# Performance work log

Measured on AMD Instinct MI355X. Metric: run time of the kernel, lower is better.

The kernel has to match this reference:

```python
import jax, jax.numpy as jnp
import numpy as np

T, B = 128, 4096          # rollout length, num parallel envs
H = 128                   # lstm hidden
FEAT = 96                 # 32 (image) + 32 (loc) + 32 (energy)
NA = 6                    # num_actions
GRID, MAXE = 10.0, 200.0


def setup_inputs() -> dict:
    key = jax.random.key(0)
    ks = jax.random.split(key, 24)
    N = T * B
    w = lambda k, shp, s=0.05: (jax.random.normal(k, shp, jnp.float32) * s)
    return {
        "image": jax.random.uniform(ks[0], (N, 5, 5), jnp.float32),
        "location": jax.random.uniform(ks[1], (N, 2), jnp.float32),
        "energy": jax.random.uniform(ks[2], (N, 1), jnp.float32),
        "done": jax.random.randint(ks[3], (N,), 0, 2).astype(jnp.int32),
        "h0": jnp.zeros((B, H), jnp.float32),
        "c0": jnp.zeros((B, H), jnp.float32),
        # visual encoder MLP 25->256->256->128->32
        "W1": w(ks[4], (25, 256)),  "b1": jnp.zeros(256, jnp.float32),
        "W2": w(ks[5], (256, 256)), "b2": jnp.zeros(256, jnp.float32),
        "W3": w(ks[6], (256, 128)), "b3": jnp.zeros(128, jnp.float32),
        "W4": w(ks[7], (128, 32)),  "b4": jnp.zeros(32, jnp.float32),
        # location / energy encoders
        "Wl": w(ks[8], (2, 32)), "bl": jnp.zeros(32, jnp.float32),
        "We": w(ks[9], (1, 32)), "be": jnp.zeros(32, jnp.float32),
        # LSTM (PyTorch layout: gates [i,f,g,o], W_ih: [4H, in], W_hh: [4H, H])
        "Wih": w(ks[10], (4 * H, FEAT)), "Whh": w(ks[11], (4 * H, H)),
        "bih": jnp.zeros(4 * H, jnp.float32), "bhh": jnp.zeros(4 * H, jnp.float32),
        # actor / critic heads
        "Wa": w(ks[12], (H, NA)), "ba": jnp.zeros(NA, jnp.float32),
        "Wc": w(ks[13], (H, 1)),  "bc": jnp.zeros(1, jnp.float32),
    }


def _forward(image, location, energy, done, h0, c0,
             W1, b1, W2, b2, W3, b3, W4, b4, Wl, bl, We, be,
             Wih, Whh, bih, bhh, Wa, ba, Wc, bc):
    relu = jax.nn.relu
    x = image.reshape(-1, 25) / 255.0                      # [N,25]
    f = relu(x @ W1 + b1)
    f = relu(f @ W2 + b2)
    f = relu(f @ W3 + b3)
    img_feat = relu(f @ W4 + b4)                           # [N,32]
    loc_feat = (location / GRID) @ Wl + bl                 # [N,32]
    eng_feat = (energy / MAXE) @ We + be                   # [N,32]
    feats = jnp.concatenate([img_feat, loc_feat, eng_feat], axis=1)  # [N,96]
    xs = feats.reshape(T, B, FEAT)
    ds = done.astype(jnp.float32).reshape(T, B)
    bias = bih + bhh                                       # [4H]

    def step(carry, inp):
        h, c = carry                                       # [B,H]
        x_t, d_t = inp
        mask = (1.0 - d_t)[:, None]                        # reset on done
        h = h * mask
        c = c * mask
        gates = x_t @ Wih.T + h @ Whh.T + bias             # [B,4H]
        i, fg, g, o = jnp.split(gates, 4, axis=1)
        c = jax.nn.sigmoid(fg) * c + jax.nn.sigmoid(i) * jnp.tanh(g)
        h = jax.nn.sigmoid(o) * jnp.tanh(c)
        return (h, c), h

    (hT, cT), hs = jax.lax.scan(step, (h0, c0), (xs, ds))  # hs: [T,B,H]
    hidden = hs.reshape(-1, H)                             # [N,H]
    logits = hidden @ Wa + ba                              # [N,NA]
    value = hidden @ Wc + bc                               # [N,1]
    return jnp.concatenate([logits, value], axis=1)        # [N,NA+1]


def reference(image, location, energy, done, h0, c0,
              W1, b1, W2, b2, W3, b3, W4, b4, Wl, bl, We, be,
              Wih, Whh, bih, bhh, Wa, ba, Wc, bc):
    return _forward(image, location, energy, done, h0, c0,
                    W1, b1, W2, b2, W3, b3, W4, b4, Wl, bl, We, be,
                    Wih, Whh, bih, bhh, Wa, ba, Wc, bc)
```

## Files before the change

### kernel.cpp

```cpp
#include <hip/hip_runtime.h>

#define T_ 128
#define B_ 4096
#define N_ (T_*B_)
#define H_ 128
#define FEAT_ 96
#define K_ 224
#define G4H_ 512
#define L2E 1.4426950408889634f

typedef __attribute__((ext_vector_type(8))) short short8;
typedef __attribute__((ext_vector_type(4))) short short4v;
typedef __attribute__((ext_vector_type(4))) float f32x4;

__device__ __forceinline__ void bar_lgkm() {
    asm volatile("s_waitcnt lgkmcnt(0)\n\ts_barrier" ::: "memory");
}

__device__ __forceinline__ short f2bf(float f) {
    unsigned r;
    asm("v_cvt_pk_bf16_f32 %0, %1, %2" : "=v"(r) : "v"(f), "v"(f));
    return (short)(r & 0xffff);
}
__device__ __forceinline__ short4v pack4relu(const f32x4 a) {
    const float x0 = fmaxf(a[0], 0.f), x1 = fmaxf(a[1], 0.f);
    const float x2 = fmaxf(a[2], 0.f), x3 = fmaxf(a[3], 0.f);
    unsigned r01, r23;
    asm("v_cvt_pk_bf16_f32 %0, %1, %2" : "=v"(r01) : "v"(x0), "v"(x1));
    asm("v_cvt_pk_bf16_f32 %0, %1, %2" : "=v"(r23) : "v"(x2), "v"(x3));
    uint2 u; u.x = r01; u.y = r23;
    return __builtin_bit_cast(short4v, u);
}

#define FBASE(t, grp, kk) ((((size_t)(t) * 256 + (grp)) * 3 + (kk)) * 512)

__global__ __launch_bounds__(256) void prep_kernel(
    const float* __restrict__ Wih, const float* __restrict__ Whh,
    const float* __restrict__ bih, const float* __restrict__ bhh,
    const float* __restrict__ W1, const float* __restrict__ W2,
    const float* __restrict__ W3, const float* __restrict__ W4,
    short* __restrict__ Wtp, float* __restrict__ bias,
    short* __restrict__ W1p, short* __restrict__ W2p,
    short* __restrict__ W3p, short* __restrict__ W4p)
{
    int idx = blockIdx.x * 256 + threadIdx.x;
    if (idx < 114688) {
        int j = idx & 7, L = (idx >> 3) & 63, r = idx >> 9;
        int kk = r % 7, n = r / 7;
        int k = kk * 32 + ((L >> 4) << 3) + j;
        int g = (n << 4) + (L & 15);
        float v = (k < FEAT_) ? Wih[g * FEAT_ + k] : Whh[g * H_ + (k - FEAT_)];
        float s = (n >= 16 && n < 24) ? (2.0f * L2E) : L2E;
        Wtp[idx] = f2bf(v * s);
        return;
    }
    int e = idx - 114688;
    if (e < 8192) {
        int j = e & 7, L = (e >> 3) & 63, nt = e >> 9;
        int k = ((L >> 4) << 3) + j;
        int o = nt * 16 + (L & 15);
        W1p[e] = (k < 25) ? f2bf(W1[k * 256 + o] * (1.0f / 255.0f)) : (short)0;
        return;
    }
    e -= 8192;
    if (e < 65536) {
        int j = e & 7, L = (e >> 3) & 63, f = e >> 9;
        int kk = f & 7, nt = f >> 3;
        int k = kk * 32 + ((L >> 4) << 3) + j;
        W2p[e] = f2bf(W2[k * 256 + nt * 16 + (L & 15)]);
        return;
    }
    e -= 65536;
    if (e < 32768) {
        int j = e & 7, L = (e >> 3) & 63, f = e >> 9;
        int kk = f & 7, nt = f >> 3;
        int k = kk * 32 + ((L >> 4) << 3) + j;
        W3p[e] = f2bf(W3[k * 128 + nt * 16 + (L & 15)]);
        return;
    }
    e -= 32768;
    if (e < 4096) {
        int j = e & 7, L = (e >> 3) & 63, f = e >> 9;
        int kk = f & 3, nt = f >> 2;
        int k = kk * 32 + ((L >> 4) << 3) + j;
        W4p[e] = f2bf(W4[k * 32 + nt * 16 + (L & 15)]);
        return;
    }
    e -= 4096;
    if (e < 512) {
        float s = ((e >> 7) == 2) ? (2.0f * L2E) : L2E;
        bias[e] = (bih[e] + bhh[e]) * s;
    }
}

__global__ __launch_bounds__(512, 1) void enc_kernel(
    const float* __restrict__ image,
    const float* __restrict__ location, const float* __restrict__ energy,
    const float* __restrict__ Wl, const float* __restrict__ bl,
    const float* __restrict__ We, const float* __restrict__ be,
    const short* __restrict__ W1p, const float* __restrict__ b1,
    const short* __restrict__ W2p, const float* __restrict__ b2,
    const short* __restrict__ W3p, const float* __restrict__ b3,
    const short* __restrict__ W4p, const float* __restrict__ b4,
    short* __restrict__ featsb)
{
    __shared__ __align__(16) float Raw[2][1600];
    __shared__ __align__(16) float LocE[2][192];
    __shared__ float C[160];
    __shared__ __align__(16) short In[4 * 512];
    __shared__ __align__(16) short AA[4 * 8 * 512];
    __shared__ __align__(16) short AB[4 * 8 * 512];
    __shared__ __align__(16) short AC[4 * 4 * 512];
    const int tid  = threadIdx.x;
    const int lane = tid & 63, wv = tid >> 6;
    const int col  = lane & 15, quad = lane >> 4;

    short8 w1r[2], w2r[2][8], w3r[8], w4r[4];
    #pragma unroll
    for (int i = 0; i < 2; i++)
        w1r[i] = *(const short8*)&W1p[((wv + 8 * i) * 64 + lane) * 8];
    #pragma unroll
    for (int i = 0; i < 2; i++)
        #pragma unroll
        for (int kk = 0; kk < 8; kk++)
            w2r[i][kk] = *(const short8*)&W2p[(((wv + 8 * i) * 8 + kk) * 64 + lane) * 8];
    #pragma unroll
    for (int kk = 0; kk < 8; kk++)
        w3r[kk] = *(const short8*)&W3p[((wv * 8 + kk) * 64 + lane) * 8];
    #pragma unroll
    for (int kk = 0; kk < 4; kk++)
        w4r[kk] = *(const short8*)&W4p[(((wv & 1) * 4 + kk) * 64 + lane) * 8];
    float4 b1r[2], b2r[2];
    #pragma unroll
    for (int i = 0; i < 2; i++) {
        b1r[i] = *(const float4*)(b1 + (wv + 8 * i) * 16 + quad * 4);
        b2r[i] = *(const float4*)(b2 + (wv + 8 * i) * 16 + quad * 4);
    }
    const float4 b3r = *(const float4*)(b3 + wv * 16 + quad * 4);
    const float4 b4r = *(const float4*)(b4 + (wv & 1) * 16 + quad * 4);

    if (tid < 160) {
        float v;
        if (tid < 64)       v = Wl[tid];
        else if (tid < 96)  v = bl[tid - 64];
        else if (tid < 128) v = We[tid - 96];
        else                v = be[tid - 128];
        C[tid] = v;
    }

    const bool ld = tid < 400;
    const int le = tid - 400;
    float4 ir = {0.f, 0.f, 0.f, 0.f};
    float4 lr = {0.f, 0.f, 0.f, 0.f};

    const int fj0 = (tid & 1) * 4;
    const int fL  = (tid >> 1) & 63;
    const int fst = tid >> 7;
    const int fs  = fst * 16 + (fL & 15);
    const int fkb = (fL >> 4) * 8 + fj0;

    auto LOCF = [&](int tl, int buf) {
        const int bi  = tid & 15;
        const int Lhi = (tid >> 4) & 3;
        const int stx = (tid >> 6) & 3;
        const int kkx = tid >> 8;
        const int s   = stx * 16 + bi;
        const float lx = LocE[buf][2 * s]     * 0.1f;
        const float ly = LocE[buf][2 * s + 1] * 0.1f;
        const float ev = LocE[buf][128 + s]   * (1.0f / 200.0f);
        const int t4l  = tl >> 6;
        const int grpl = (tl & 63) * 4 + stx;
        short8 v;
        #pragma unroll
        for (int j = 0; j < 8; j++) {
            const int kl = Lhi * 8 + j;
            float val;
            if (kkx == 0) val = fmaf(lx, C[kl], fmaf(ly, C[32 + kl], C[64 + kl]));
            else          val = fmaf(ev, C[96 + kl], C[128 + kl]);
            v[j] = f2bf(val);
        }
        *(short8*)&featsb[FBASE(t4l, grpl, 1 + kkx) + (Lhi * 16 + bi) * 8] = v;
    };

    if (ld) {
        *(float4*)&Raw[0][4 * tid] = *(const float4*)(image + (size_t)blockIdx.x * 1600 + 4 * tid);
        ir = *(const float4*)(image + (size_t)(blockIdx.x + 256) * 1600 + 4 * tid);
    } else if (le < 48) {
        const float* s0 = (le < 32) ? (location + (size_t)blockIdx.x * 128 + 4 * le)
                                    : (energy   + (size_t)blockIdx.x * 64  + 4 * (le - 32));
        const float* s1 = (le < 32) ? (location + (size_t)(blockIdx.x + 256) * 128 + 4 * le)
                                    : (energy   + (size_t)(blockIdx.x + 256) * 64  + 4 * (le - 32));
        *(float4*)&LocE[0][4 * le] = *(const float4*)s0;
        lr = *(const float4*)s1;
    }
    bar_lgkm();
    {
        short4v v;
        #pragma unroll
        for (int jj = 0; jj < 4; jj++) {
            const int kx = fkb + jj;
            v[jj] = (kx < 25) ? f2bf(Raw[0][fs * 25 + kx]) : (short)0;
        }
        *(short4v*)&In[(fst * 64 + fL) * 8 + fj0] = v;
    }
    LOCF(blockIdx.x, 0);

    for (int it = 0; it < 32; it++) {
        const int nxt = (it & 1) ^ 1;
        const int tile = it * 256 + blockIdx.x;
        if (it + 1 < 32) {
            if (ld) *(float4*)&Raw[nxt][4 * tid] = ir;
            else if (le < 48) *(float4*)&LocE[nxt][4 * le] = lr;
        }
        if (it + 2 < 32) {
            if (ld) ir = *(const float4*)(image + (size_t)(tile + 512) * 1600 + 4 * tid);
            else if (le < 48) {
                const float* s1 = (le < 32) ? (location + (size_t)(tile + 512) * 128 + 4 * le)
                                            : (energy   + (size_t)(tile + 512) * 64  + 4 * (le - 32));
                lr = *(const float4*)s1;
            }
        }
        bar_lgkm();

        {
            short8 bx[4];
            #pragma unroll
            for (int st = 0; st < 4; st++) bx[st] = *(const short8*)&In[(st * 64 + lane) * 8];
            #pragma unroll
            for (int i = 0; i < 2; i++) {
                const int nt = wv + 8 * i;
                #pragma unroll
                for (int st = 0; st < 4; st++) {
                    f32x4 acc = (f32x4){b1r[i].x, b1r[i].y, b1r[i].z, b1r[i].w};
                    acc = __builtin_amdgcn_mfma_f32_16x16x32_bf16(w1r[i], bx[st], acc, 0, 0, 0);
                    *(short4v*)&AA[((st * 8 + (nt >> 1)) * 64 + ((((nt & 1) << 1) + (quad >> 1)) << 4) + col) * 8 + (quad & 1) * 4]
                        = pack4relu(acc);
                }
            }
        }
        bar_lgkm();

        {
            f32x4 acc[2][4];
            #pragma unroll
            for (int i = 0; i < 2; i++)
                #pragma unroll
                for (int st = 0; st < 4; st++)
                    acc[i][st] = (f32x4){b2r[i].x, b2r[i].y, b2r[i].z, b2r[i].w};
            #pragma unroll
            for (int kk = 0; kk < 8; kk++) {
                short8 bx[4];
                #pragma unroll
                for (int st = 0; st < 4; st++)
                    bx[st] = *(const short8*)&AA[((st * 8 + kk) * 64 + lane) * 8];
                #pragma unroll
                for (int i = 0; i < 2; i++)
                    #pragma unroll
                    for (int st = 0; st < 4; st++)
                        acc[i][st] = __builtin_amdgcn_mfma_f32_16x16x32_bf16(w2r[i][kk], bx[st], acc[i][st], 0, 0, 0);
            }
            #pragma unroll
            for (int i = 0; i < 2; i++) {
                const int nt = wv + 8 * i;
                #pragma unroll
                for (int st = 0; st < 4; st++)
                    *(short4v*)&AB[((st * 8 + (nt >> 1)) * 64 + ((((nt & 1) << 1) + (quad >> 1)) << 4) + col) * 8 + (quad & 1) * 4]
                        = pack4relu(acc[i][st]);
            }
        }
        bar_lgkm();

        {
            f32x4 acc[4];
            #pragma unroll
            for (int st = 0; st < 4; st++) acc[st] = (f32x4){b3r.x, b3r.y, b3r.z, b3r.w};
            #pragma unroll
            for (int kk = 0; kk < 8; kk++) {
                #pragma unroll
                for (int st = 0; st < 4; st++) {
                    const short8 bx = *(const short8*)&AB[((st * 8 + kk) * 64 + lane) * 8];
                    acc[st] = __builtin_amdgcn_mfma_f32_16x16x32_bf16(w3r[kk], bx, acc[st], 0, 0, 0);
                }
            }
            const int nt = wv;
            #pragma unroll
            for (int st = 0; st < 4; st++)
                *(short4v*)&AC[((st * 4 + (nt >> 1)) * 64 + ((((nt & 1) << 1) + (quad >> 1)) << 4) + col) * 8 + (quad & 1) * 4]
                    = pack4relu(acc[st]);
        }
        bar_lgkm();

        {
            const int nt = wv & 1, st = wv >> 1;
            f32x4 acc = (f32x4){b4r.x, b4r.y, b4r.z, b4r.w};
            #pragma unroll
            for (int kk = 0; kk < 4; kk++) {
                const short8 bx = *(const short8*)&AC[((st * 4 + kk) * 64 + lane) * 8];
                acc = __builtin_amdgcn_mfma_f32_16x16x32_bf16(w4r[kk], bx, acc, 0, 0, 0);
            }
            const int t4 = tile >> 6;
            const int grp = (tile & 63) * 4 + st;
            *(short4v*)&featsb[FBASE(t4, grp, 0) + (((nt << 1) + (quad >> 1)) * 16 + col) * 8 + (quad & 1) * 4]
                = pack4relu(acc);
        }
        if (it + 1 < 32) {
            LOCF(tile + 256, nxt);
            short4v v;
            #pragma unroll
            for (int jj = 0; jj < 4; jj++) {
                const int kx = fkb + jj;
                v[jj] = (kx < 25) ? f2bf(Raw[nxt][fs * 25 + kx]) : (short)0;
            }
            *(short4v*)&In[(fst * 64 + fL) * 8 + fj0] = v;
        }
    }
}

__global__ __launch_bounds__(512, 1) void lstm_kernel(
    const short* __restrict__ featsb, const int* __restrict__ done,
    const float* __restrict__ h0, const float* __restrict__ c0,
    const short* __restrict__ Wtp, const float* __restrict__ bias,
    const float* __restrict__ Wa, const float* __restrict__ ba,
    const float* __restrict__ Wc, const float* __restrict__ bc,
    float* __restrict__ out)
{
    __shared__ __align__(16) short Hb[2][4 * 64 * 8];
    __shared__ __align__(16) short HW[4 * 64 * 8];
    __shared__ float Ml[T_ * 16];

    const int tid = threadIdx.x;
    const int r0 = blockIdx.x * 16;
    const int grp = r0 >> 4;
    const int lane = tid & 63;
    const int wv = tid >> 6;
    const int col = lane & 15;
    const int quad = lane >> 4;
    const int u = (wv << 4) + col;

    short8 wtr[4][7];
    #pragma unroll
    for (int g = 0; g < 4; g++)
        #pragma unroll
        for (int kk = 0; kk < 7; kk++)
            wtr[g][kk] = *(const short8*)&Wtp[((size_t)((wv + 8 * g) * 7 + kk) * 64 + lane) * 8];

    for (int idx = tid; idx < 4 * 64 * 8; idx += 512) {
        int j = idx & 7, L = (idx >> 3) & 63, kk2 = idx >> 9;
        int k = kk2 * 32 + ((L >> 4) << 3) + j;
        int n = L & 15;
        float v = (n < 6) ? Wa[k * 6 + n] : (n == 6 ? Wc[k] : 0.0f);
        HW[idx] = f2bf(v);
    }
    for (int idx = tid; idx < T_ * 16; idx += 512)
        Ml[idx] = 1.0f - (float)done[(size_t)(idx >> 4) * B_ + r0 + (idx & 15)];

    const int kk2h = wv >> 1;
    const int Lhi_h = ((wv & 1) << 1) | (col >> 3);
    const int jh = col & 7;
    f32x4 c;
    #pragma unroll
    for (int r = 0; r < 4; r++) {
        const int s = (quad << 2) + r;
        const float m = 1.0f - (float)done[r0 + s];
        c[r] = c0[(size_t)(r0 + s) * H_ + u] * m;
        Hb[0][(kk2h * 64 + Lhi_h * 16 + s) * 8 + jh] = f2bf(h0[(size_t)(r0 + s) * H_ + u]);
    }
    const float bi0 = bias[((wv +  0) << 4) + col];
    const float bi1 = bias[((wv +  8) << 4) + col];
    const float bi2 = bias[((wv + 16) << 4) + col];
    const float bi3 = bias[((wv + 24) << 4) + col];
    const float hb = (col < 6) ? ba[col] : (col == 6 ? bc[0] : 0.0f);

    short8 xa[3], xb[3];
    #pragma unroll
    for (int kk = 0; kk < 3; kk++) {
        xa[kk] = *(const short8*)&featsb[FBASE(0, grp, kk) + lane * 8];
        xb[kk] = *(const short8*)&featsb[FBASE(1, grp, kk) + lane * 8];
    }
    f32x4 axA[4], axB[4];
    axA[0] = (f32x4){bi0, bi0, bi0, bi0};
    axA[1] = (f32x4){bi1, bi1, bi1, bi1};
    axA[2] = (f32x4){bi2, bi2, bi2, bi2};
    axA[3] = (f32x4){bi3, bi3, bi3, bi3};
    #pragma unroll
    for (int kk = 0; kk < 3; kk++) {
        axA[0] = __builtin_amdgcn_mfma_f32_16x16x32_bf16(xa[kk], wtr[0][kk], axA[0], 0, 0, 0);
        axA[1] = __builtin_amdgcn_mfma_f32_16x16x32_bf16(xa[kk], wtr[1][kk], axA[1], 0, 0, 0);
        axA[2] = __builtin_amdgcn_mfma_f32_16x16x32_bf16(xa[kk], wtr[2][kk], axA[2], 0, 0, 0);
        axA[3] = __builtin_amdgcn_mfma_f32_16x16x32_bf16(xa[kk], wtr[3][kk], axA[3], 0, 0, 0);
    }
    bar_lgkm();

    auto STEP = [&](int t, int cur, short8* Xload, short8* Xuse, f32x4* axT, f32x4* axN) {
        const int nxt = cur ^ 1;
        if (t + 2 < T_) {
            #pragma unroll
            for (int kk = 0; kk < 3; kk++)
                Xload[kk] = *(const short8*)&featsb[FBASE(t + 2, grp, kk) + lane * 8];
        }
        const float mcol = Ml[t * 16 + col];
        f32x4 acc0 = axT[0], acc1 = axT[1], acc2 = axT[2], acc3 = axT[3];
        #pragma unroll
        for (int kk2 = 0; kk2 < 4; kk2++) {
            short8 af = *(const short8*)&Hb[cur][(kk2 * 64 + lane) * 8];
            if (mcol == 0.0f) af = (short8){0,0,0,0,0,0,0,0};
            acc0 = __builtin_amdgcn_mfma_f32_16x16x32_bf16(af, wtr[0][3 + kk2], acc0, 0, 0, 0);
            acc1 = __builtin_amdgcn_mfma_f32_16x16x32_bf16(af, wtr[1][3 + kk2], acc1, 0, 0, 0);
            acc2 = __builtin_amdgcn_mfma_f32_16x16x32_bf16(af, wtr[2][3 + kk2], acc2, 0, 0, 0);
            acc3 = __builtin_amdgcn_mfma_f32_16x16x32_bf16(af, wtr[3][3 + kk2], acc3, 0, 0, 0);
        }
        f32x4 n0 = (f32x4){bi0, bi0, bi0, bi0};
        f32x4 n1 = (f32x4){bi1, bi1, bi1, bi1};
        f32x4 n2 = (f32x4){bi2, bi2, bi2, bi2};
        f32x4 n3 = (f32x4){bi3, bi3, bi3, bi3};
        #pragma unroll
        for (int kk = 0; kk < 3; kk++) {
            n0 = __builtin_amdgcn_mfma_f32_16x16x32_bf16(Xuse[kk], wtr[0][kk], n0, 0, 0, 0);
            n1 = __builtin_amdgcn_mfma_f32_16x16x32_bf16(Xuse[kk], wtr[1][kk], n1, 0, 0, 0);
            n2 = __builtin_amdgcn_mfma_f32_16x16x32_bf16(Xuse[kk], wtr[2][kk], n2, 0, 0, 0);
            n3 = __builtin_amdgcn_mfma_f32_16x16x32_bf16(Xuse[kk], wtr[3][kk], n3, 0, 0, 0);
        }
        axN[0] = n0; axN[1] = n1; axN[2] = n2; axN[3] = n3;
        float4 mn = {1.f, 1.f, 1.f, 1.f};
        if (t < T_ - 1) mn = *(const float4*)&Ml[(t + 1) * 16 + (quad << 2)];
        #pragma unroll
        for (int r = 0; r < 4; r++) {
            const float ei = __builtin_amdgcn_exp2f(-acc0[r]);
            const float ef = __builtin_amdgcn_exp2f(-acc1[r]);
            const float eg = __builtin_amdgcn_exp2f(-acc2[r]);
            const float eo = __builtin_amdgcn_exp2f(-acc3[r]);
            const float Ai = 1.0f + ei, Bf = 1.0f + ef;
            const float Gg = 1.0f + eg, Do = 1.0f + eo;
            const float AG = Ai * Gg;
            const float num = fmaf(c[r], AG, (1.0f - eg) * Bf);
            const float cn = num * __builtin_amdgcn_rcpf(AG * Bf);
            const float et = __builtin_amdgcn_exp2f(-2.0f * L2E * cn);
            const float h = (1.0f - et) * __builtin_amdgcn_rcpf(Do * (1.0f + et));
            c[r] = cn * ((&mn.x)[r]);
            Hb[nxt][(kk2h * 64 + Lhi_h * 16 + (quad << 2) + r) * 8 + jh] = f2bf(h);
        }
        bar_lgkm();

        if (wv == (t & 7)) {
            f32x4 ha = {hb, hb, hb, hb};
            #pragma unroll
            for (int kk2 = 0; kk2 < 4; kk2++) {
                const short8 hf = *(const short8*)&Hb[nxt][(kk2 * 64 + lane) * 8];
                const short8 wf = *(const short8*)&HW[(kk2 * 64 + lane) * 8];
                ha = __builtin_amdgcn_mfma_f32_16x16x32_bf16(hf, wf, ha, 0, 0, 0);
            }
            if (col < 7) {
                #pragma unroll
                for (int r = 0; r < 4; r++) {
                    const int s = (quad << 2) + r;
                    out[((size_t)t * B_ + r0 + s) * 7 + col] = ha[r];
                }
            }
        }
    };

    for (int t = 0; t < T_; t += 2) {
        STEP(t,     0, xa, xb, axA, axB);
        STEP(t + 1, 1, xb, xa, axB, axA);
    }
}

extern "C" void kernel_launch(void* const* d_in, const int* in_sizes, int n_in,
                              void* d_out, int out_size, void* d_ws, size_t ws_size,
                              hipStream_t stream) {
    const float* image    = (const float*)d_in[0];
    const float* location = (const float*)d_in[1];
    const float* energy   = (const float*)d_in[2];
    const int*   done     = (const int*)d_in[3];
    const float* h0       = (const float*)d_in[4];
    const float* c0       = (const float*)d_in[5];
    const float* W1 = (const float*)d_in[6];   const float* b1 = (const float*)d_in[7];
    const float* W2 = (const float*)d_in[8];   const float* b2 = (const float*)d_in[9];
    const float* W3 = (const float*)d_in[10];  const float* b3 = (const float*)d_in[11];
    const float* W4 = (const float*)d_in[12];  const float* b4 = (const float*)d_in[13];
    const float* Wl = (const float*)d_in[14];  const float* bl = (const float*)d_in[15];
    const float* We = (const float*)d_in[16];  const float* be = (const float*)d_in[17];
    const float* Wih = (const float*)d_in[18]; const float* Whh = (const float*)d_in[19];
    const float* bih = (const float*)d_in[20]; const float* bhh = (const float*)d_in[21];
    const float* Wa = (const float*)d_in[22];  const float* ba = (const float*)d_in[23];
    const float* Wc = (const float*)d_in[24];  const float* bc = (const float*)d_in[25];

    char* ws = (char*)d_ws;
    short* Wtp   = (short*)ws;
    float* bias  = (float*)(ws + 229376);
    short* W1p   = (short*)(ws + 231424);
    short* W2p   = (short*)(ws + 247808);
    short* W3p   = (short*)(ws + 378880);
    short* W4p   = (short*)(ws + 444416);
    short* featsb = (short*)(ws + 452608);
    float* out   = (float*)d_out;

    prep_kernel<<<882, 256, 0, stream>>>(Wih, Whh, bih, bhh, W1, W2, W3, W4,
                                         Wtp, bias, W1p, W2p, W3p, W4p);
    enc_kernel<<<256, 512, 0, stream>>>(image, location, energy, Wl, bl, We, be,
                                        W1p, b1, W2p, b2, W3p, b3, W4p, b4, featsb);
    lstm_kernel<<<B_ / 16, 512, 0, stream>>>(featsb, done, h0, c0, Wtp, bias,
                                             Wa, ba, Wc, bc, out);
}
```

Measured before the change: 389.4 us.

## Software-pipeline encoder MLP layers across tiles to cut barriers per iteration

```diff
diff --git a/kernel.cpp b/kernel.cpp
--- a/kernel.cpp
+++ b/kernel.cpp
@@ -181,6 +181,46 @@
         }
         *(short8*)&featsb[FBASE(t4l, grpl, 1 + kkx) + (Lhi * 16 + bi) * 8] = v;
     };
+    auto FRAG = [&](int buf) {
+        short4v v;
+        #pragma unroll
+        for (int jj = 0; jj < 4; jj++) {
+            const int kx = fkb + jj;
+            v[jj] = (kx < 25) ? f2bf(Raw[buf][fs * 25 + kx]) : (short)0;
+        }
+        *(short4v*)&In[(fst * 64 + fL) * 8 + fj0] = v;
+    };
+    auto L3B = [&]() {
+        f32x4 acc[4];
+        #pragma unroll
+        for (int st = 0; st < 4; st++) acc[st] = (f32x4){b3r.x, b3r.y, b3r.z, b3r.w};
+        #pragma unroll
+        for (int kk = 0; kk < 8; kk++) {
+            #pragma unroll
+            for (int st = 0; st < 4; st++) {
+                const short8 bx = *(const short8*)&AB[((st * 8 + kk) * 64 + lane) * 8];
+                acc[st] = __builtin_amdgcn_mfma_f32_16x16x32_bf16(w3r[kk], bx, acc[st], 0, 0, 0);
+            }
+        }
+        const int nt = wv;
+        #pragma unroll
+        for (int st = 0; st < 4; st++)
+            *(short4v*)&AC[((st * 4 + (nt >> 1)) * 64 + ((((nt & 1) << 1) + (quad >> 1)) << 4) + col) * 8 + (quad & 1) * 4]
+                = pack4relu(acc[st]);
+    };
+    auto L4B = [&](int pt) {
+        const int nt = wv & 1, st = wv >> 1;
+        f32x4 acc = (f32x4){b4r.x, b4r.y, b4r.z, b4r.w};
+        #pragma unroll
+        for (int kk = 0; kk < 4; kk++) {
+            const short8 bx = *(const short8*)&AC[((st * 4 + kk) * 64 + lane) * 8];
+            acc = __builtin_amdgcn_mfma_f32_16x16x32_bf16(w4r[kk], bx, acc, 0, 0, 0);
+        }
+        const int t4 = pt >> 6;
+        const int grp = (pt & 63) * 4 + st;
+        *(short4v*)&featsb[FBASE(t4, grp, 0) + (((nt << 1) + (quad >> 1)) * 16 + col) * 8 + (quad & 1) * 4]
+            = pack4relu(acc);
+    };
 
     if (ld) {
         *(float4*)&Raw[0][4 * tid] = *(const float4*)(image + (size_t)blockIdx.x * 1600 + 4 * tid);
@@ -194,16 +234,9 @@
         lr = *(const float4*)s1;
     }
     bar_lgkm();
-    {
-        short4v v;
-        #pragma unroll
-        for (int jj = 0; jj < 4; jj++) {
-            const int kx = fkb + jj;
-            v[jj] = (kx < 25) ? f2bf(Raw[0][fs * 25 + kx]) : (short)0;
-        }
-        *(short4v*)&In[(fst * 64 + fL) * 8 + fj0] = v;
-    }
+    FRAG(0);
     LOCF(blockIdx.x, 0);
+    bar_lgkm();
 
     for (int it = 0; it < 32; it++) {
         const int nxt = (it & 1) ^ 1;
@@ -220,8 +253,6 @@
                 lr = *(const float4*)s1;
             }
         }
-        bar_lgkm();
-
         {
             short8 bx[4];
             #pragma unroll
@@ -238,6 +269,7 @@
                 }
             }
         }
+        if (it >= 1) L3B();
         bar_lgkm();
 
         {
@@ -268,52 +300,16 @@
                         = pack4relu(acc[i][st]);
             }
         }
-        bar_lgkm();
-
-        {
-            f32x4 acc[4];
-            #pragma unroll
-            for (int st = 0; st < 4; st++) acc[st] = (f32x4){b3r.x, b3r.y, b3r.z, b3r.w};
-            #pragma unroll
-            for (int kk = 0; kk < 8; kk++) {
-                #pragma unroll
-                for (int st = 0; st < 4; st++) {
-                    const short8 bx = *(const short8*)&AB[((st * 8 + kk) * 64 + lane) * 8];
-                    acc[st] = __builtin_amdgcn_mfma_f32_16x16x32_bf16(w3r[kk], bx, acc[st], 0, 0, 0);
-                }
-            }
-            const int nt = wv;
-            #pragma unroll
-            for (int st = 0; st < 4; st++)
-                *(short4v*)&AC[((st * 4 + (nt >> 1)) * 64 + ((((nt & 1) << 1) + (quad >> 1)) << 4) + col) * 8 + (quad & 1) * 4]
-                    = pack4relu(acc[st]);
-        }
-        bar_lgkm();
-
-        {
-            const int nt = wv & 1, st = wv >> 1;
-            f32x4 acc = (f32x4){b4r.x, b4r.y, b4r.z, b4r.w};
-            #pragma unroll
-            for (int kk = 0; kk < 4; kk++) {
-                const short8 bx = *(const short8*)&AC[((st * 4 + kk) * 64 + lane) * 8];
-                acc = __builtin_amdgcn_mfma_f32_16x16x32_bf16(w4r[kk], bx, acc, 0, 0, 0);
-            }
-            const int t4 = tile >> 6;
-            const int grp = (tile & 63) * 4 + st;
-            *(short4v*)&featsb[FBASE(t4, grp, 0) + (((nt << 1) + (quad >> 1)) * 16 + col) * 8 + (quad & 1) * 4]
-                = pack4relu(acc);
-        }
+        if (it >= 1) L4B(tile - 256);
         if (it + 1 < 32) {
             LOCF(tile + 256, nxt);
-            short4v v;
-            #pragma unroll
-            for (int jj = 0; jj < 4; jj++) {
-                const int kx = fkb + jj;
-                v[jj] = (kx < 25) ? f2bf(Raw[nxt][fs * 25 + kx]) : (short)0;
-            }
-            *(short4v*)&In[(fst * 64 + fL) * 8 + fj0] = v;
-        }
-    }
+            FRAG(nxt);
+        }
+        bar_lgkm();
+    }
+    L3B();
+    bar_lgkm();
+    L4B(31 * 256 + blockIdx.x);
 }
 
 __global__ __launch_bounds__(512, 1) void lstm_kernel(
```

New measurement: 385.9 us. Within noise of the previous version (-0.9%).
